# Optimization experiments

Measured on AMD Instinct MI355X. Metric: run time of the kernel, lower is better.

Reference implementation:

```python
import jax, jax.numpy as jnp
import numpy as np

EPS = 1e-8

def setup_inputs() -> dict:
    key = jax.random.key(0)
    k1, k2 = jax.random.split(key)
    B, N, M, D = 8, 4096, 4096, 3
    x1 = jax.random.normal(k1, (B, N, D), dtype=jnp.float32)
    y1 = jax.random.normal(k2, (B, M, D), dtype=jnp.float32)
    return {"x1": x1, "y1": y1}

def reference(x1, y1):
    # Faithful to: dist = sqrt(1e-8 + sum((x1[:,None,:,:] - y1[:,:,None,:])**2, -1))
    # computed via the Gram-matrix expansion to avoid the (B,M,N,D) intermediate.
    x_sq = jnp.sum(x1 * x1, axis=-1)                 # (B, N)
    y_sq = jnp.sum(y1 * y1, axis=-1)                 # (B, M)
    xy = jnp.einsum('bmd,bnd->bmn', y1, x1)          # (B, M, N)
    d2 = jnp.maximum(y_sq[:, :, None] + x_sq[:, None, :] - 2.0 * xy, 0.0)
    dist = jnp.sqrt(EPS + d2)                        # (B, M, N)
    min1 = jnp.min(dist, axis=1)                     # (B, N): nearest y for each x
    min2 = jnp.min(dist, axis=2)                     # (B, M): nearest x for each y
    return jnp.mean(min1) + jnp.mean(min2)
```

## Files before the change

kernel.cpp:

```cpp
#include <hip/hip_runtime.h>

constexpr int B = 8;
constexpr int N = 4096;
constexpr int PTS = B * N;
constexpr int TOT = 2 * PTS;

#define TPB 256
#define R 16
#define RP (R / 2)
#define CHUNK 128
#define KC (N / CHUNK)

typedef float float2v __attribute__((ext_vector_type(2)));

__global__ __launch_bounds__(TPB) void chamfer_min5(
        const float* __restrict__ x1, const float* __restrict__ y1,
        float* __restrict__ partials,
        float* __restrict__ out) {
    __shared__ float4 qs[CHUNK];

    if (blockIdx.x == 0 && blockIdx.y == 0 && blockIdx.z == 0 && threadIdx.x == 0)
        out[0] = 0.0f;

    const int chunk = blockIdx.x;
    const int dir   = blockIdx.y;
    const int b     = blockIdx.z;

    const float* own = dir ? y1 : x1;
    const float* oth = dir ? x1 : y1;

    if (threadIdx.x < CHUNK) {
        const float* op = oth + ((size_t)b * N + chunk * CHUNK + threadIdx.x) * 3;
        float qx = op[0], qy = op[1], qz = op[2];
        qs[threadIdx.x] = make_float4(qx, qy, qz, fmaf(qx, qx, fmaf(qy, qy, qz * qz)));
    }

    float2v mx2[RP], my2[RP], mz2[RP], acc2[RP];
    float xx[R];
    #pragma unroll
    for (int p = 0; p < RP; p++) {
        #pragma unroll
        for (int e = 0; e < 2; e++) {
            const int r = 2 * p + e;
            const float* pp = own + ((size_t)b * N + threadIdx.x + r * TPB) * 3;
            float px = pp[0], py = pp[1], pz = pp[2];
            mx2[p][e] = -2.0f * px;
            my2[p][e] = -2.0f * py;
            mz2[p][e] = -2.0f * pz;
            xx[r] = fmaf(px, px, fmaf(py, py, pz * pz));
        }
        acc2[p] = float2v{3.4e38f, 3.4e38f};
    }

    __syncthreads();

    #pragma unroll 2
    for (int j = 0; j < CHUNK; j += 2) {
        union { float4 f4; float2v f2[2]; } qa0, qa1;
        qa0.f4 = qs[j];
        qa1.f4 = qs[j + 1];
        float2v xy0 = qa0.f2[0], zw0 = qa0.f2[1];
        float2v xy1 = qa1.f2[0], zw1 = qa1.f2[1];
        #pragma unroll
        for (int p = 0; p < RP; p++) {
            float2v g0, g1;
            asm("v_pk_fma_f32 %0, %1, %2, %1 op_sel:[0,0,1] op_sel_hi:[0,1,1]"
                : "=v"(g0) : "v"(zw0), "v"(mz2[p]));
            asm("v_pk_fma_f32 %0, %1, %2, %1 op_sel:[0,0,1] op_sel_hi:[0,1,1]"
                : "=v"(g1) : "v"(zw1), "v"(mz2[p]));
            asm("v_pk_fma_f32 %0, %1, %2, %3 op_sel:[1,0,0] op_sel_hi:[1,1,1]"
                : "=v"(g0) : "v"(xy0), "v"(my2[p]), "v"(g0));
            asm("v_pk_fma_f32 %0, %1, %2, %3 op_sel:[1,0,0] op_sel_hi:[1,1,1]"
                : "=v"(g1) : "v"(xy1), "v"(my2[p]), "v"(g1));
            asm("v_pk_fma_f32 %0, %1, %2, %3 op_sel:[0,0,0] op_sel_hi:[0,1,1]"
                : "=v"(g0) : "v"(xy0), "v"(mx2[p]), "v"(g0));
            asm("v_pk_fma_f32 %0, %1, %2, %3 op_sel:[0,0,0] op_sel_hi:[0,1,1]"
                : "=v"(g1) : "v"(xy1), "v"(mx2[p]), "v"(g1));
            acc2[p].x = fminf(fminf(acc2[p].x, g0.x), g1.x);
            acc2[p].y = fminf(fminf(acc2[p].y, g0.y), g1.y);
        }
    }

    float* dst = partials + (size_t)chunk * TOT + (size_t)dir * PTS + (size_t)b * N;
    #pragma unroll
    for (int p = 0; p < RP; p++) {
        dst[threadIdx.x + (2 * p) * TPB]     = fmaxf(acc2[p].x + xx[2 * p], 0.0f);
        dst[threadIdx.x + (2 * p + 1) * TPB] = fmaxf(acc2[p].y + xx[2 * p + 1], 0.0f);
    }
}

__global__ __launch_bounds__(256) void chamfer_finish(
        const float* __restrict__ partials, float* __restrict__ out, float scale) {
    int p = blockIdx.x * 256 + threadIdx.x;
    float m = partials[p];
    #pragma unroll
    for (int c = 1; c < KC; c++) m = fminf(m, partials[(size_t)c * TOT + p]);
    float s = sqrtf(1e-8f + m) * scale;

    #pragma unroll
    for (int off = 32; off > 0; off >>= 1) s += __shfl_down(s, off, 64);

    __shared__ float partial[4];
    const int wid = threadIdx.x >> 6, lane = threadIdx.x & 63;
    if (lane == 0) partial[wid] = s;
    __syncthreads();
    if (threadIdx.x == 0) {
        atomicAdd(out, partial[0] + partial[1] + partial[2] + partial[3]);
    }
}

extern "C" void kernel_launch(void* const* d_in, const int* in_sizes, int n_in,
                              void* d_out, int out_size, void* d_ws, size_t ws_size,
                              hipStream_t stream) {
    const float* x1 = (const float*)d_in[0];
    const float* y1 = (const float*)d_in[1];
    float* out = (float*)d_out;

    float* partials = (float*)d_ws;

    dim3 grid(KC, 2, B);
    chamfer_min5<<<grid, TPB, 0, stream>>>(x1, y1, partials, out);

    chamfer_finish<<<TOT / 256, 256, 0, stream>>>(partials, out, 1.0f / (B * N));
}
```

Baseline: 82.11 us.

## Precompute query float4s in a prep kernel and read them directly from global memory

```diff
diff --git a/kernel.cpp b/kernel.cpp
--- a/kernel.cpp
+++ b/kernel.cpp
@@ -8,32 +8,33 @@
 #define TPB 256
 #define R 16
 #define RP (R / 2)
-#define CHUNK 128
-#define KC (N / CHUNK)
+#define JR 64
+#define KJ (N / JR)
 
 typedef float float2v __attribute__((ext_vector_type(2)));
 
-__global__ __launch_bounds__(TPB) void chamfer_min5(
+__global__ __launch_bounds__(256) void prep(
         const float* __restrict__ x1, const float* __restrict__ y1,
-        float* __restrict__ partials,
-        float* __restrict__ out) {
-    __shared__ float4 qs[CHUNK];
+        float4* __restrict__ qpre, float* __restrict__ out) {
+    int tid = blockIdx.x * 256 + threadIdx.x;
+    if (tid == 0) out[0] = 0.0f;
+    if (tid >= TOT) return;
+    int dir = tid >> 15;
+    int p   = tid & (PTS - 1);
+    const float* src = dir ? x1 : y1;
+    float qx = src[3 * p], qy = src[3 * p + 1], qz = src[3 * p + 2];
+    qpre[tid] = make_float4(qx, qy, qz, fmaf(qx, qx, fmaf(qy, qy, qz * qz)));
+}
 
-    if (blockIdx.x == 0 && blockIdx.y == 0 && blockIdx.z == 0 && threadIdx.x == 0)
-        out[0] = 0.0f;
-
-    const int chunk = blockIdx.x;
-    const int dir   = blockIdx.y;
-    const int b     = blockIdx.z;
+__global__ __launch_bounds__(TPB) void chamfer_main(
+        const float* __restrict__ x1, const float* __restrict__ y1,
+        const float4* __restrict__ qpre,
+        float* __restrict__ partials) {
+    const int jrange = blockIdx.x;
+    const int dir    = blockIdx.y;
+    const int b      = blockIdx.z;
 
     const float* own = dir ? y1 : x1;
-    const float* oth = dir ? x1 : y1;
-
-    if (threadIdx.x < CHUNK) {
-        const float* op = oth + ((size_t)b * N + chunk * CHUNK + threadIdx.x) * 3;
-        float qx = op[0], qy = op[1], qz = op[2];
-        qs[threadIdx.x] = make_float4(qx, qy, qz, fmaf(qx, qx, fmaf(qy, qy, qz * qz)));
-    }
 
     float2v mx2[RP], my2[RP], mz2[RP], acc2[RP];
     float xx[R];
@@ -52,15 +53,15 @@
         acc2[p] = float2v{3.4e38f, 3.4e38f};
     }
 
-    __syncthreads();
+    const float4* __restrict__ qp =
+        qpre + (size_t)dir * PTS + (size_t)b * N + (size_t)jrange * JR;
 
-    #pragma unroll 2
-    for (int j = 0; j < CHUNK; j += 2) {
-        union { float4 f4; float2v f2[2]; } qa0, qa1;
-        qa0.f4 = qs[j];
-        qa1.f4 = qs[j + 1];
-        float2v xy0 = qa0.f2[0], zw0 = qa0.f2[1];
-        float2v xy1 = qa1.f2[0], zw1 = qa1.f2[1];
+    #pragma unroll 8
+    for (int t = 0; t < JR / 2; t++) {
+        float4 qv0 = qp[2 * t];
+        float4 qv1 = qp[2 * t + 1];
+        float2v xy0 = {qv0.x, qv0.y}, zw0 = {qv0.z, qv0.w};
+        float2v xy1 = {qv1.x, qv1.y}, zw1 = {qv1.z, qv1.w};
         #pragma unroll
         for (int p = 0; p < RP; p++) {
             float2v g0, g1;
@@ -81,7 +82,7 @@
         }
     }
 
-    float* dst = partials + (size_t)chunk * TOT + (size_t)dir * PTS + (size_t)b * N;
+    float* dst = partials + (size_t)jrange * TOT + (size_t)dir * PTS + (size_t)b * N;
     #pragma unroll
     for (int p = 0; p < RP; p++) {
         dst[threadIdx.x + (2 * p) * TPB]     = fmaxf(acc2[p].x + xx[2 * p], 0.0f);
@@ -94,18 +95,18 @@
     int p = blockIdx.x * 256 + threadIdx.x;
     float m = partials[p];
     #pragma unroll
-    for (int c = 1; c < KC; c++) m = fminf(m, partials[(size_t)c * TOT + p]);
+    for (int c = 1; c < KJ; c++) m = fminf(m, partials[(size_t)c * TOT + p]);
     float s = sqrtf(1e-8f + m) * scale;
 
     #pragma unroll
     for (int off = 32; off > 0; off >>= 1) s += __shfl_down(s, off, 64);
 
-    __shared__ float partial[4];
+    __shared__ float part[4];
     const int wid = threadIdx.x >> 6, lane = threadIdx.x & 63;
-    if (lane == 0) partial[wid] = s;
+    if (lane == 0) part[wid] = s;
     __syncthreads();
     if (threadIdx.x == 0) {
-        atomicAdd(out, partial[0] + partial[1] + partial[2] + partial[3]);
+        atomicAdd(out, part[0] + part[1] + part[2] + part[3]);
     }
 }
 
@@ -116,10 +117,13 @@
     const float* y1 = (const float*)d_in[1];
     float* out = (float*)d_out;
 
-    float* partials = (float*)d_ws;
+    float4* qpre    = (float4*)d_ws;
+    float* partials = (float*)(qpre + TOT);
 
-    dim3 grid(KC, 2, B);
-    chamfer_min5<<<grid, TPB, 0, stream>>>(x1, y1, partials, out);
+    prep<<<TOT / 256, 256, 0, stream>>>(x1, y1, qpre, out);
+
+    dim3 grid(KJ, 2, B);
+    chamfer_main<<<grid, TPB, 0, stream>>>(x1, y1, qpre, partials);
 
     chamfer_finish<<<TOT / 256, 256, 0, stream>>>(partials, out, 1.0f / (B * N));
 }
```

Result: slower. 92.12 us (+12.2%).
